# Kernel tuning notes

Measured on AMD Instinct MI355X. Metric: run time of the kernel, lower is better.

Reference implementation:

```python
import jax, jax.numpy as jnp
import numpy as np

B, S, D, H = 2, 2048, 1024, 16
DK = D // H
ROPE_BASE = 10000.0


def _rope_tables(seq_len, dim):
    # [S, dim] cos/sin tables, matching torch cat([freqs, freqs], -1)
    inv_freq = 1.0 / (ROPE_BASE ** (jnp.arange(0, dim, 2, dtype=jnp.float32) / dim))
    freqs = jnp.arange(seq_len, dtype=jnp.float32)[:, None] * inv_freq[None, :]
    emb = jnp.concatenate([freqs, freqs], axis=-1)
    return jnp.cos(emb), jnp.sin(emb)


def _rotate_half(x):
    x1, x2 = x[..., : x.shape[-1] // 2], x[..., x.shape[-1] // 2 :]
    return jnp.concatenate([-x2, x1], axis=-1)


def setup_inputs() -> dict:
    key = jax.random.key(0)
    ks = jax.random.split(key, 8)
    q = jax.random.normal(ks[0], (B, S, D), jnp.float32)
    k = jax.random.normal(ks[1], (B, S, D), jnp.float32)
    v = jax.random.normal(ks[2], (B, S, D), jnp.float32)
    mask = jnp.tril(jnp.ones((S, S), jnp.int32))[None, None]  # causal [1,1,S,S]
    scale = 0.02
    Wq = jax.random.normal(ks[3], (D, D), jnp.float32) * scale
    Wk = jax.random.normal(ks[4], (D, D), jnp.float32) * scale
    Wv = jax.random.normal(ks[5], (D, D), jnp.float32) * scale
    Wo = jax.random.normal(ks[6], (D, D), jnp.float32) * scale
    bq = jnp.zeros((D,), jnp.float32)
    bk = jnp.zeros((D,), jnp.float32)
    bv = jnp.zeros((D,), jnp.float32)
    bo = jnp.zeros((D,), jnp.float32)
    return {"q": q, "k": k, "v": v, "mask": mask,
            "Wq": Wq, "bq": bq, "Wk": Wk, "bk": bk,
            "Wv": Wv, "bv": bv, "Wo": Wo, "bo": bo}


def reference(q, k, v, mask, Wq, bq, Wk, bk, Wv, bv, Wo, bo):
    b, s, d = q.shape
    # QKV projections, reshape to [B, H, S, d_k]
    query = (q @ Wq + bq).reshape(b, s, H, DK).transpose(0, 2, 1, 3)
    key_ = (k @ Wk + bk).reshape(b, s, H, DK).transpose(0, 2, 1, 3)
    value = (v @ Wv + bv).reshape(b, s, H, DK).transpose(0, 2, 1, 3)
    # RoPE on q and k
    cos, sin = _rope_tables(s, DK)  # [S, DK]
    cos = cos[None, None]
    sin = sin[None, None]
    query = query * cos + _rotate_half(query) * sin
    key_ = key_ * cos + _rotate_half(key_) * sin
    # scaled dot-product attention with mask-fill
    scores = jnp.einsum("bhqd,bhkd->bhqk", query, key_) / jnp.sqrt(jnp.float32(DK))
    scores = jnp.where(mask == 0, jnp.float32(-1e9), scores)
    attn = jax.nn.softmax(scores, axis=-1)
    out = jnp.einsum("bhqk,bhkd->bhqd", attn, value)  # [B,H,S,DK]
    out = out.transpose(0, 2, 1, 3).reshape(b, s, d)
    return out @ Wo + bo
```

## Files before the change

kernel.cpp:

```cpp
#include <hip/hip_runtime.h>
#include <hip/hip_bf16.h>
#include <math.h>

#define Bb 2
#define Ss 2048
#define Dd 1024
#define Hh 16
#define DKk 64
#define BSn (Bb*Ss)

typedef unsigned short u16;
typedef __attribute__((ext_vector_type(8))) short frag_ab;
typedef __attribute__((ext_vector_type(4))) float frag_cd;

static __device__ __forceinline__ u16 f2bf(float x) {
    __hip_bfloat16 h = __float2bfloat16(x);
    return *reinterpret_cast<u16*>(&h);
}

static __device__ __forceinline__ void gload16(const u16* g, u16* l) {
    __builtin_amdgcn_global_load_lds(
        (const __attribute__((address_space(1))) void*)g,
        (__attribute__((address_space(3))) void*)l, 16, 0, 0);
}

__global__ __launch_bounds__(256)
void convert_kernel(const float* __restrict__ q, const float* __restrict__ k,
                    const float* __restrict__ v,
                    const float* __restrict__ Wq, const float* __restrict__ Wk,
                    const float* __restrict__ Wv, const float* __restrict__ Wo,
                    u16* __restrict__ qb, u16* __restrict__ kb, u16* __restrict__ vb,
                    u16* __restrict__ wqt, u16* __restrict__ wkt,
                    u16* __restrict__ wvt, u16* __restrict__ wot)
{
    __shared__ u16 T[64 * 80];
    const int tid = threadIdx.x;
    const int bid = blockIdx.x;
    if (bid < 3072) {
        int t = bid >> 10;
        const float* src = (t == 0) ? q : (t == 1) ? k : v;
        u16* dst = (t == 0) ? qb : (t == 1) ? kb : vb;
        size_t base = (size_t)(bid & 1023) * 4096;
#pragma unroll
        for (int i = 0; i < 4; ++i) {
            size_t e = base + (size_t)(tid + i * 256) * 4;
            float4 xv = *(const float4*)(src + e);
            ushort4 o;
            o.x = f2bf(xv.x); o.y = f2bf(xv.y); o.z = f2bf(xv.z); o.w = f2bf(xv.w);
            *(ushort4*)(dst + e) = o;
        }
    } else {
        int wbid = bid - 3072;
        int w = wbid >> 8;
        const float* src = (w == 0) ? Wq : (w == 1) ? Wk : (w == 2) ? Wv : Wo;
        u16* dst = (w == 0) ? wqt : (w == 1) ? wkt : (w == 2) ? wvt : wot;
        int t = wbid & 255;
        int k0 = (t >> 4) * 64, nt0 = (t & 15) * 64;
#pragma unroll
        for (int i = 0; i < 4; ++i) {
            int f = tid + i * 256;
            int kk = f >> 4, nn = (f & 15) * 4;
            float4 xv = *(const float4*)(src + (size_t)(k0 + kk) * Dd + nt0 + nn);
            T[(nn + 0) * 80 + kk] = f2bf(xv.x);
            T[(nn + 1) * 80 + kk] = f2bf(xv.y);
            T[(nn + 2) * 80 + kk] = f2bf(xv.z);
            T[(nn + 3) * 80 + kk] = f2bf(xv.w);
        }
        __syncthreads();
#pragma unroll
        for (int i = 0; i < 2; ++i) {
            int g = tid + i * 256;
            int nn = g >> 3, k8 = (g & 7) * 8;
            *(uint4*)(dst + (size_t)(nt0 + nn) * Dd + k0 + k8) =
                *(const uint4*)&T[nn * 80 + k8];
        }
    }
}

__global__ __launch_bounds__(256)
void gemm_bf16(const u16* __restrict__ X0, const u16* __restrict__ X1,
               const u16* __restrict__ X2,
               const u16* __restrict__ W0, const u16* __restrict__ W1,
               const u16* __restrict__ W2,
               const float* __restrict__ b0, const float* __restrict__ b1,
               const float* __restrict__ b2,
               u16* __restrict__ O0, u16* __restrict__ O1, u16* __restrict__ O2,
               float* __restrict__ OutF, int fused)
{
    __shared__ u16 As[128 * 64];
    __shared__ u16 Bs[64 * 64];

    const int tid = threadIdx.x;
    const int wv = tid >> 6, lane = tid & 63, l16 = lane & 15, quad = lane >> 4;
    const int n0 = blockIdx.x * 64, m0 = blockIdx.y * 128;
    const int z = blockIdx.z;

    const u16* X      = fused ? ((z == 0) ? X0 : (z == 1) ? X1 : X2) : X0;
    const u16* Wt     = fused ? ((z == 0) ? W0 : (z == 1) ? W1 : W2) : W0;
    const float* bias = fused ? ((z == 0) ? b0 : (z == 1) ? b1 : b2) : b0;
    u16* OutB         = (z == 0) ? O0 : (z == 1) ? O1 : O2;
    const int mode    = fused ? ((z == 0) ? 1 : (z == 1) ? 3 : 2) : 0;

    const int srow = tid >> 3;
    const int scol = (tid & 7) * 8;

    frag_cd acc[2][4];
#pragma unroll
    for (int ms = 0; ms < 2; ++ms)
#pragma unroll
        for (int n = 0; n < 4; ++n) acc[ms][n] = (frag_cd){0.f, 0.f, 0.f, 0.f};

    for (int k0 = 0; k0 < Dd; k0 += 64) {
        __syncthreads();
#pragma unroll
        for (int p = 0; p < 4; ++p)
            gload16(&X[(size_t)(m0 + p * 32 + srow) * Dd + k0 + scol],
                    &As[p * 2048 + wv * 512]);
#pragma unroll
        for (int p = 0; p < 2; ++p)
            gload16(&Wt[(size_t)(n0 + p * 32 + srow) * Dd + k0 + scol],
                    &Bs[p * 2048 + wv * 512]);
        __syncthreads();

#pragma unroll
        for (int ks = 0; ks < 2; ++ks) {
            frag_ab a0 = *(const frag_ab*)&As[(wv * 32 + l16) * 64 + ks * 32 + quad * 8];
            frag_ab a1 = *(const frag_ab*)&As[(wv * 32 + 16 + l16) * 64 + ks * 32 + quad * 8];
#pragma unroll
            for (int n = 0; n < 4; ++n) {
                frag_ab b = *(const frag_ab*)&Bs[(n * 16 + l16) * 64 + ks * 32 + quad * 8];
                acc[0][n] = __builtin_amdgcn_mfma_f32_16x16x32_bf16(a0, b, acc[0][n], 0, 0, 0);
                acc[1][n] = __builtin_amdgcn_mfma_f32_16x16x32_bf16(a1, b, acc[1][n], 0, 0, 0);
            }
        }
    }

    float bv4[4];
#pragma unroll
    for (int n = 0; n < 4; ++n) bv4[n] = bias[n0 + n * 16 + l16];

    if (mode == 0) {
#pragma unroll
        for (int ms = 0; ms < 2; ++ms)
#pragma unroll
            for (int r = 0; r < 4; ++r) {
                int row = m0 + wv * 32 + ms * 16 + quad * 4 + r;
#pragma unroll
                for (int n = 0; n < 4; ++n)
                    OutF[(size_t)row * Dd + n0 + n * 16 + l16] = acc[ms][n][r] + bv4[n];
            }
    } else if (mode == 2) {
        const int h = n0 >> 6;
        const int b = m0 >> 11;
#pragma unroll
        for (int ms = 0; ms < 2; ++ms) {
            int sbase = (m0 & (Ss - 1)) + wv * 32 + ms * 16 + quad * 4;
#pragma unroll
            for (int n = 0; n < 4; ++n) {
                int d = n * 16 + l16;
                ushort4 o;
                o.x = f2bf(acc[ms][n][0] + bv4[n]);
                o.y = f2bf(acc[ms][n][1] + bv4[n]);
                o.z = f2bf(acc[ms][n][2] + bv4[n]);
                o.w = f2bf(acc[ms][n][3] + bv4[n]);
                *(ushort4*)&OutB[(((size_t)b * Hh + h) * DKk + d) * Ss + sbase] = o;
            }
        }
    } else {
        const int h = n0 >> 6;
        const float lg = 0.28782313662425575f;
        const float sc = (mode == 1) ? 0.125f : 1.0f;
#pragma unroll
        for (int ms = 0; ms < 2; ++ms)
#pragma unroll
            for (int r = 0; r < 4; ++r) {
                int row = m0 + wv * 32 + ms * 16 + quad * 4 + r;
                int b = row >> 11, s = row & (Ss - 1);
                u16* orow = OutB + (((size_t)b * Hh + h) * Ss + s) * DKk;
#pragma unroll
                for (int n = 0; n < 2; ++n) {
                    int j = n * 16 + l16;
                    float ang = (float)s * __expf(-(float)j * lg);
                    float cv = cosf(ang), sv = sinf(ang);
                    float lo = acc[ms][n][r] + bv4[n];
                    float hi = acc[ms][n + 2][r] + bv4[n + 2];
                    orow[j]      = f2bf((lo * cv - hi * sv) * sc);
                    orow[j + 32] = f2bf((hi * cv + lo * sv) * sc);
                }
            }
    }
}

__global__ __launch_bounds__(256)
void gemm_out(const u16* __restrict__ X0, const u16* __restrict__ W0,
              const float* __restrict__ b0, float* __restrict__ OutF)
{
    __shared__ u16 As[64 * 64];
    __shared__ u16 Bs[64 * 64];

    const int tid = threadIdx.x;
    const int wv = tid >> 6, lane = tid & 63, l16 = lane & 15, quad = lane >> 4;
    const int n0 = blockIdx.x * 64, m0 = blockIdx.y * 64;

    const int srow = tid >> 3;
    const int scol = (tid & 7) * 8;

    frag_cd acc[4];
#pragma unroll
    for (int n = 0; n < 4; ++n) acc[n] = (frag_cd){0.f, 0.f, 0.f, 0.f};

    for (int k0 = 0; k0 < Dd; k0 += 64) {
        __syncthreads();
#pragma unroll
        for (int p = 0; p < 2; ++p) {
            gload16(&X0[(size_t)(m0 + p * 32 + srow) * Dd + k0 + scol],
                    &As[p * 2048 + wv * 512]);
            gload16(&W0[(size_t)(n0 + p * 32 + srow) * Dd + k0 + scol],
                    &Bs[p * 2048 + wv * 512]);
        }
        __syncthreads();

#pragma unroll
        for (int ks = 0; ks < 2; ++ks) {
            frag_ab a0 = *(const frag_ab*)&As[(wv * 16 + l16) * 64 + ks * 32 + quad * 8];
#pragma unroll
            for (int n = 0; n < 4; ++n) {
                frag_ab b = *(const frag_ab*)&Bs[(n * 16 + l16) * 64 + ks * 32 + quad * 8];
                acc[n] = __builtin_amdgcn_mfma_f32_16x16x32_bf16(a0, b, acc[n], 0, 0, 0);
            }
        }
    }

    float bv4[4];
#pragma unroll
    for (int n = 0; n < 4; ++n) bv4[n] = b0[n0 + n * 16 + l16];

#pragma unroll
    for (int r = 0; r < 4; ++r) {
        int row = m0 + wv * 16 + quad * 4 + r;
#pragma unroll
        for (int n = 0; n < 4; ++n)
            OutF[(size_t)row * Dd + n0 + n * 16 + l16] = acc[n][r] + bv4[n];
    }
}

__global__ __launch_bounds__(256)
void attn_mfma(const u16* __restrict__ Q, const u16* __restrict__ K,
               const u16* __restrict__ Vt, u16* __restrict__ Aout)
{
    __shared__ u16 Ks[2][64 * 64];
    __shared__ u16 Vs[2][64 * 64];
    __shared__ u16 Ps[64 * 64];

    const int tid = threadIdx.x;
    const int wv = tid >> 6;
    const int lane = tid & 63;
    const int l16 = lane & 15;
    const int quad = lane >> 4;

    const int bh = blockIdx.y;
    const int vsw = (blockIdx.x + (bh & 7)) & 31;
    const int jj  = bh >> 3;
    const int qb  = (jj == 0) ? vsw
                  : (jj == 1) ? ((vsw + 8) & 31)
                  : (jj == 2) ? ((23 - vsw) & 31)
                  :             (31 - vsw);
    const int q0 = qb * 64;

    const size_t qkbase = (size_t)bh * Ss * DKk;
    const size_t vbase  = (size_t)bh * DKk * Ss;
    const int b = bh >> 4, h = bh & 15;

    const int srow = tid >> 3;
    const int scol = ((tid & 7) ^ (srow & 7)) * 8;
    const int sx   = (l16 & 7) * 8;

    frag_ab qreg[2];
    {
        const u16* qrow = &Q[qkbase + (size_t)(q0 + wv * 16 + l16) * DKk];
#pragma unroll
        for (int h2 = 0; h2 < 2; ++h2)
            qreg[h2] = *(const frag_ab*)&qrow[h2 * 32 + quad * 8];
    }

#pragma unroll
    for (int p = 0; p < 2; ++p) {
        gload16(&K[qkbase + (size_t)(p * 32 + srow) * DKk + scol],
                &Ks[0][p * 2048 + wv * 512]);
        gload16(&Vt[vbase + (size_t)(p * 32 + srow) * Ss + scol],
                &Vs[0][p * 2048 + wv * 512]);
    }

    float m_r = -3.0e38f, l_r = 0.f;
    frag_cd of[4];
#pragma unroll
    for (int n = 0; n < 4; ++n) of[n] = (frag_cd){0.f, 0.f, 0.f, 0.f};

    for (int kb = 0; kb <= qb; ++kb) {
        const int cur = kb & 1;
        const u16* KsB = Ks[cur];
        const u16* VsB = Vs[cur];

        __syncthreads();

        if (kb < qb) {
            const int k0n = (kb + 1) * 64;
#pragma unroll
            for (int p = 0; p < 2; ++p) {
                gload16(&K[qkbase + (size_t)(k0n + p * 32 + srow) * DKk + scol],
                        &Ks[cur ^ 1][p * 2048 + wv * 512]);
                gload16(&Vt[vbase + (size_t)(p * 32 + srow) * Ss + k0n + scol],
                        &Vs[cur ^ 1][p * 2048 + wv * 512]);
            }
        }

        frag_cd sf[4];
#pragma unroll
        for (int n = 0; n < 4; ++n) sf[n] = (frag_cd){0.f, 0.f, 0.f, 0.f};
#pragma unroll
        for (int h2 = 0; h2 < 2; ++h2) {
#pragma unroll
            for (int n = 0; n < 4; ++n) {
                frag_ab kf = *(const frag_ab*)&KsB[(n * 16 + l16) * 64 + ((h2 * 32 + quad * 8) ^ sx)];
                sf[n] = __builtin_amdgcn_mfma_f32_16x16x32_bf16(kf, qreg[h2], sf[n], 0, 0, 0);
            }
        }

        if (kb == qb) {
            const int qloc = wv * 16 + l16;
#pragma unroll
            for (int n = 0; n < 4; ++n)
#pragma unroll
                for (int r = 0; r < 4; ++r)
                    if (n * 16 + quad * 4 + r > qloc) sf[n][r] = -1.0e30f;
        }

        frag_cd t0, t1;
#pragma unroll
        for (int r = 0; r < 4; ++r) {
            t0[r] = fmaxf(sf[0][r], sf[1][r]);
            t1[r] = fmaxf(sf[2][r], sf[3][r]);
        }
        float mx = fmaxf(fmaxf(fmaxf(t0[0], t1[0]), fmaxf(t0[1], t1[1])),
                         fmaxf(fmaxf(t0[2], t1[2]), fmaxf(t0[3], t1[3])));
        mx = fmaxf(mx, m_r);
        mx = fmaxf(mx, __shfl_xor(mx, 16));
        mx = fmaxf(mx, __shfl_xor(mx, 32));

        float a = __expf(m_r - mx);
        m_r = mx;

        frag_cd s0, s1;
#pragma unroll
        for (int n = 0; n < 4; ++n)
#pragma unroll
            for (int r = 0; r < 4; ++r)
                sf[n][r] = __expf(sf[n][r] - mx);
#pragma unroll
        for (int r = 0; r < 4; ++r) {
            s0[r] = sf[0][r] + sf[1][r];
            s1[r] = sf[2][r] + sf[3][r];
        }
        float sum = ((s0[0] + s1[0]) + (s0[1] + s1[1])) +
                    ((s0[2] + s1[2]) + (s0[3] + s1[3]));
        sum += __shfl_xor(sum, 16);
        sum += __shfl_xor(sum, 32);
        l_r = l_r * a + sum;

        float a4[4];
#pragma unroll
        for (int r = 0; r < 4; ++r)
            a4[r] = __shfl(a, (lane & 48) | (quad * 4 + r));
#pragma unroll
        for (int n = 0; n < 4; ++n)
#pragma unroll
            for (int r = 0; r < 4; ++r) of[n][r] *= a4[r];

        {
            const int prow = wv * 16 + l16;
            const int px8  = (l16 & 7) << 3;
#pragma unroll
            for (int n = 0; n < 4; ++n) {
                ushort4 o;
                o.x = f2bf(sf[n][0]); o.y = f2bf(sf[n][1]);
                o.z = f2bf(sf[n][2]); o.w = f2bf(sf[n][3]);
                *(ushort4*)&Ps[prow * 64 + ((n * 16 + quad * 4) ^ px8)] = o;
            }
        }
        __threadfence_block();

#pragma unroll
        for (int h2 = 0; h2 < 2; ++h2) {
            frag_ab pa = *(const frag_ab*)&Ps[(wv * 16 + l16) * 64 + ((h2 * 32 + quad * 8) ^ sx)];
#pragma unroll
            for (int n = 0; n < 4; ++n) {
                frag_ab vf = *(const frag_ab*)&VsB[(n * 16 + l16) * 64 + ((h2 * 32 + quad * 8) ^ sx)];
                of[n] = __builtin_amdgcn_mfma_f32_16x16x32_bf16(pa, vf, of[n], 0, 0, 0);
            }
        }
    }

    float linv = 1.f / l_r;
    float inv4[4];
#pragma unroll
    for (int r = 0; r < 4; ++r)
        inv4[r] = __shfl(linv, (lane & 48) | (quad * 4 + r));

#pragma unroll
    for (int r = 0; r < 4; ++r) {
        int row = q0 + wv * 16 + quad * 4 + r;
        u16* orow = Aout + ((size_t)b * Ss + row) * Dd + h * DKk;
#pragma unroll
        for (int n = 0; n < 4; ++n) orow[n * 16 + l16] = f2bf(of[n][r] * inv4[r]);
    }
}

extern "C" void kernel_launch(void* const* d_in, const int* in_sizes, int n_in,
                              void* d_out, int out_size, void* d_ws, size_t ws_size,
                              hipStream_t stream) {
    (void)in_sizes; (void)n_in; (void)out_size;
    const float* q  = (const float*)d_in[0];
    const float* k  = (const float*)d_in[1];
    const float* v  = (const float*)d_in[2];
    const float* Wq = (const float*)d_in[4];
    const float* bq = (const float*)d_in[5];
    const float* Wk = (const float*)d_in[6];
    const float* bk = (const float*)d_in[7];
    const float* Wv = (const float*)d_in[8];
    const float* bv = (const float*)d_in[9];
    const float* Wo = (const float*)d_in[10];
    const float* bo = (const float*)d_in[11];
    float* out = (float*)d_out;

    const size_t E = (size_t)Bb * Ss * Dd;
    const size_t Wn = (size_t)Dd * Dd;
    const size_t need = (7 * E + 4 * Wn) * sizeof(u16);
    if (ws_size < need) return;
    u16* qa  = (u16*)d_ws;
    u16* ka  = qa + E;
    u16* va  = ka + E;
    u16* wqt = va + E;
    u16* wkt = wqt + Wn;
    u16* wvt = wkt + Wn;
    u16* wot = wvt + Wn;
    u16* Qh  = wot + Wn;
    u16* Kh  = Qh + E;
    u16* Vth = Kh + E;
    u16* Abf = Vth + E;

    convert_kernel<<<4096, 256, 0, stream>>>(q, k, v, Wq, Wk, Wv, Wo,
                                             qa, ka, va, wqt, wkt, wvt, wot);
    gemm_bf16<<<dim3(Dd / 64, BSn / 128, 3), 256, 0, stream>>>(
        qa, ka, va, wqt, wkt, wvt, bq, bk, bv, Qh, Kh, Vth, nullptr, 1);
    attn_mfma<<<dim3(32, Bb * Hh), 256, 0, stream>>>(Qh, Kh, Vth, Abf);
    gemm_out<<<dim3(Dd / 64, BSn / 64), 256, 0, stream>>>(Abf, wot, bo, out);
}
```

Measured before the change: 268.6 us.

## Split long causal attention rows across two blocks with a merge kernel

Query blocks in the upper half of the causal range now have their key range split into two halves, each processed by its own workgroup. The grid grows from 32 to 48 blocks per head so the work per block is more even. Partial outputs and row max/sum statistics go to fp32 scratch, reusing the converted-input workspace, and a new merge kernel combines them with log-sum-exp rescaling. This aims to shorten the critical path set by the longest causal rows, at the cost of an extra launch and extra global traffic for the partials.

```diff
diff --git a/kernel.cpp b/kernel.cpp
--- a/kernel.cpp
+++ b/kernel.cpp
@@ -246,7 +246,8 @@
 
 __global__ __launch_bounds__(256)
 void attn_mfma(const u16* __restrict__ Q, const u16* __restrict__ K,
-               const u16* __restrict__ Vt, u16* __restrict__ Aout)
+               const u16* __restrict__ Vt, u16* __restrict__ Aout,
+               float* __restrict__ ofP, float* __restrict__ mlP)
 {
     __shared__ u16 Ks[2][64 * 64];
     __shared__ u16 Vs[2][64 * 64];
@@ -259,13 +260,12 @@
     const int quad = lane >> 4;
 
     const int bh = blockIdx.y;
-    const int vsw = (blockIdx.x + (bh & 7)) & 31;
-    const int jj  = bh >> 3;
-    const int qb  = (jj == 0) ? vsw
-                  : (jj == 1) ? ((vsw + 8) & 31)
-                  : (jj == 2) ? ((23 - vsw) & 31)
-                  :             (31 - vsw);
-    const int q0 = qb * 64;
+    const int x = (blockIdx.x + bh * 5) % 48;
+    int q, kb0, kb1, half;
+    if (x < 32) { q = x; kb0 = 0; kb1 = (x < 16) ? x : 15; half = 0; }
+    else        { q = x - 16; kb0 = 16; kb1 = q; half = 1; }
+    const int split = (q >= 16);
+    const int q0 = q * 64;
 
     const size_t qkbase = (size_t)bh * Ss * DKk;
     const size_t vbase  = (size_t)bh * DKk * Ss;
@@ -283,12 +283,15 @@
             qreg[h2] = *(const frag_ab*)&qrow[h2 * 32 + quad * 8];
     }
 
-#pragma unroll
-    for (int p = 0; p < 2; ++p) {
-        gload16(&K[qkbase + (size_t)(p * 32 + srow) * DKk + scol],
-                &Ks[0][p * 2048 + wv * 512]);
-        gload16(&Vt[vbase + (size_t)(p * 32 + srow) * Ss + scol],
-                &Vs[0][p * 2048 + wv * 512]);
+    {
+        const int k0p = kb0 * 64;
+#pragma unroll
+        for (int p = 0; p < 2; ++p) {
+            gload16(&K[qkbase + (size_t)(k0p + p * 32 + srow) * DKk + scol],
+                    &Ks[0][p * 2048 + wv * 512]);
+            gload16(&Vt[vbase + (size_t)(p * 32 + srow) * Ss + k0p + scol],
+                    &Vs[0][p * 2048 + wv * 512]);
+        }
     }
 
     float m_r = -3.0e38f, l_r = 0.f;
@@ -296,14 +299,16 @@
 #pragma unroll
     for (int n = 0; n < 4; ++n) of[n] = (frag_cd){0.f, 0.f, 0.f, 0.f};
 
-    for (int kb = 0; kb <= qb; ++kb) {
-        const int cur = kb & 1;
+    const int nkb = kb1 - kb0 + 1;
+    for (int i = 0; i < nkb; ++i) {
+        const int kb = kb0 + i;
+        const int cur = i & 1;
         const u16* KsB = Ks[cur];
         const u16* VsB = Vs[cur];
 
         __syncthreads();
 
-        if (kb < qb) {
+        if (i < nkb - 1) {
             const int k0n = (kb + 1) * 64;
 #pragma unroll
             for (int p = 0; p < 2; ++p) {
@@ -326,7 +331,7 @@
             }
         }
 
-        if (kb == qb) {
+        if (kb == q) {
             const int qloc = wv * 16 + l16;
 #pragma unroll
             for (int n = 0; n < 4; ++n)
@@ -400,18 +405,70 @@
         }
     }
 
-    float linv = 1.f / l_r;
-    float inv4[4];
-#pragma unroll
-    for (int r = 0; r < 4; ++r)
-        inv4[r] = __shfl(linv, (lane & 48) | (quad * 4 + r));
-
-#pragma unroll
-    for (int r = 0; r < 4; ++r) {
-        int row = q0 + wv * 16 + quad * 4 + r;
-        u16* orow = Aout + ((size_t)b * Ss + row) * Dd + h * DKk;
-#pragma unroll
-        for (int n = 0; n < 4; ++n) orow[n * 16 + l16] = f2bf(of[n][r] * inv4[r]);
+    if (!split) {
+        float linv = 1.f / l_r;
+        float inv4[4];
+#pragma unroll
+        for (int r = 0; r < 4; ++r)
+            inv4[r] = __shfl(linv, (lane & 48) | (quad * 4 + r));
+#pragma unroll
+        for (int r = 0; r < 4; ++r) {
+            int row = q0 + wv * 16 + quad * 4 + r;
+            u16* orow = Aout + ((size_t)b * Ss + row) * Dd + h * DKk;
+#pragma unroll
+            for (int n = 0; n < 4; ++n) orow[n * 16 + l16] = f2bf(of[n][r] * inv4[r]);
+        }
+    } else {
+        const size_t pbase = (((size_t)bh * 16 + (q - 16)) * 2 + half) * 4096;
+#pragma unroll
+        for (int r = 0; r < 4; ++r) {
+            int row = wv * 16 + quad * 4 + r;
+#pragma unroll
+            for (int n = 0; n < 4; ++n)
+                ofP[pbase + (size_t)row * 64 + n * 16 + l16] = of[n][r];
+        }
+        if (quad == 0) {
+            const size_t mb = (((size_t)bh * 16 + (q - 16)) * 2 + half) * 128;
+            mlP[mb + wv * 16 + l16]      = m_r;
+            mlP[mb + 64 + wv * 16 + l16] = l_r;
+        }
+    }
+}
+
+__global__ __launch_bounds__(256)
+void attn_merge(const float* __restrict__ ofP, const float* __restrict__ mlP,
+                u16* __restrict__ Aout)
+{
+    const int s = blockIdx.x;
+    const int bh = blockIdx.y;
+    const int tid = threadIdx.x;
+    const int row = tid >> 2;
+    const int c0  = (tid & 3) * 16;
+    const int b = bh >> 4, h = bh & 15;
+    const int q0 = (s + 16) * 64;
+
+    const size_t baseA = (((size_t)bh * 16 + s) * 2 + 0) * 4096 + (size_t)row * 64;
+    const size_t baseB = baseA + 4096;
+    const size_t mbA = (((size_t)bh * 16 + s) * 2 + 0) * 128;
+    const size_t mbB = mbA + 128;
+
+    float mA = mlP[mbA + row], lA = mlP[mbA + 64 + row];
+    float mB = mlP[mbB + row], lB = mlP[mbB + 64 + row];
+    float m  = fmaxf(mA, mB);
+    float aA = __expf(mA - m), aB = __expf(mB - m);
+    float inv = 1.f / (lA * aA + lB * aB);
+
+    u16* orow = Aout + ((size_t)b * Ss + q0 + row) * Dd + h * DKk;
+#pragma unroll
+    for (int j4 = 0; j4 < 4; ++j4) {
+        float4 vA = *(const float4*)&ofP[baseA + c0 + j4 * 4];
+        float4 vB = *(const float4*)&ofP[baseB + c0 + j4 * 4];
+        ushort4 o;
+        o.x = f2bf((vA.x * aA + vB.x * aB) * inv);
+        o.y = f2bf((vA.y * aA + vB.y * aB) * inv);
+        o.z = f2bf((vA.z * aA + vB.z * aB) * inv);
+        o.w = f2bf((vA.w * aA + vB.w * aB) * inv);
+        *(ushort4*)&orow[c0 + j4 * 4] = o;
     }
 }
 
@@ -448,10 +505,14 @@
     u16* Vth = Kh + E;
     u16* Abf = Vth + E;
 
+    float* ofP = (float*)qa;
+    float* mlP = (float*)va;
+
     convert_kernel<<<4096, 256, 0, stream>>>(q, k, v, Wq, Wk, Wv, Wo,
                                              qa, ka, va, wqt, wkt, wvt, wot);
     gemm_bf16<<<dim3(Dd / 64, BSn / 128, 3), 256, 0, stream>>>(
         qa, ka, va, wqt, wkt, wvt, bq, bk, bv, Qh, Kh, Vth, nullptr, 1);
-    attn_mfma<<<dim3(32, Bb * Hh), 256, 0, stream>>>(Qh, Kh, Vth, Abf);
+    attn_mfma<<<dim3(48, Bb * Hh), 256, 0, stream>>>(Qh, Kh, Vth, Abf, ofP, mlP);
+    attn_merge<<<dim3(16, Bb * Hh), 256, 0, stream>>>(ofP, mlP, Abf);
     gemm_out<<<dim3(Dd / 64, BSn / 64), 256, 0, stream>>>(Abf, wot, bo, out);
 }
```

Measured after the change: 262.4 us. 2.3% less time.
